# Kernel tuning notes

Measured on AMD Instinct MI355X. Metric: run time of the kernel, lower is better.

Reference implementation:

```python
import jax, jax.numpy as jnp
import numpy as np

VOXEL_SIZE = 0.05  # from init_kwargs


def _voxel_ds(pts, voxel_size, key, L):
    """Voxel-grid downsample one cloud (N,3): mean of points per occupied voxel,
    then resample L voxel centroids (uniform with replacement among valid voxels).
    Static shapes throughout (jit/vmap friendly)."""
    N = pts.shape[0]
    mn = jnp.min(pts, axis=0)
    v = jnp.floor((pts - mn) / voxel_size).astype(jnp.int32)      # (N,3) voxel coords >= 0
    dims = jnp.max(v, axis=0) + 1                                  # traced grid extents
    lin = (v[:, 0] * dims[1] + v[:, 1]) * dims[2] + v[:, 2]        # linearized voxel id
    order = jnp.argsort(lin)
    sl = lin[order]
    is_new = jnp.concatenate([jnp.ones((1,), bool), sl[1:] != sl[:-1]])
    seg = jnp.cumsum(is_new) - 1                                   # compact segment id per sorted point
    num_vox = seg[-1] + 1                                          # traced count of occupied voxels
    sums = jax.ops.segment_sum(pts[order], seg, num_segments=N)    # (N,3) padded
    cnt = jax.ops.segment_sum(jnp.ones((N,), pts.dtype), seg, num_segments=N)
    means = sums / jnp.maximum(cnt, 1.0)[:, None]                  # voxel centroids
    # random resample L centroids among the first num_vox valid segments
    u = jax.random.uniform(key, (L,))
    idx = jnp.minimum((u * num_vox.astype(u.dtype)).astype(jnp.int32), num_vox - 1)
    return means[idx]                                              # (L,3)


def _voxel_layer(x, voxel_size, L, key):
    # x: (B,3,N) -> (B,3,L)
    B = x.shape[0]
    pts = jnp.transpose(x, (0, 2, 1))                              # (B,N,3)
    keys = jax.random.split(key, B)
    out = jax.vmap(lambda p, k: _voxel_ds(p, voxel_size, k, L))(pts, keys)
    return jnp.transpose(out, (0, 2, 1))                           # (B,3,L)


def setup_inputs() -> dict:
    key = jax.random.key(0)
    x = jax.random.uniform(key, (16, 3, 262144), dtype=jnp.float32)
    return {"x": x}


def reference(x):
    B, _, N = x.shape
    L1, L2 = N // 2, N // 4
    k1, k2 = jax.random.split(jax.random.key(42))
    voxel_x1 = _voxel_layer(x, VOXEL_SIZE, L1, k1)
    voxel_x2 = _voxel_layer(voxel_x1, 2.0 * VOXEL_SIZE, L2, k2)
    return (voxel_x1, voxel_x2)
```

## Files before the change

### kernel.cpp

```cpp
#include <hip/hip_runtime.h>
#include <stdint.h>


typedef unsigned int u32;
typedef unsigned long long u64;

struct KeyArr { uint32_t k0[16]; uint32_t k1[16]; };

__host__ __device__ inline void tf2x32(uint32_t k0, uint32_t k1,
                                       uint32_t c0, uint32_t c1,
                                       uint32_t& o0, uint32_t& o1) {
  const uint32_t ks0 = k0, ks1 = k1, ks2 = k0 ^ k1 ^ 0x1BD11BDAu;
  uint32_t x0 = c0 + ks0, x1 = c1 + ks1;
#define TF_R(r) { x0 += x1; x1 = (x1 << (r)) | (x1 >> (32 - (r))); x1 ^= x0; }
  TF_R(13) TF_R(15) TF_R(26) TF_R(6)
  x0 += ks1; x1 += ks2 + 1u;
  TF_R(17) TF_R(29) TF_R(16) TF_R(24)
  x0 += ks2; x1 += ks0 + 2u;
  TF_R(13) TF_R(15) TF_R(26) TF_R(6)
  x0 += ks0; x1 += ks1 + 3u;
  TF_R(17) TF_R(29) TF_R(16) TF_R(24)
  x0 += ks1; x1 += ks2 + 4u;
  TF_R(13) TF_R(15) TF_R(26) TF_R(6)
  x0 += ks2; x1 += ks0 + 5u;
#undef TF_R
  o0 = x0; o1 = x1;
}

__global__ void init_kernel(u64* cellsA, u64* cellsB, int ncells) {
  int i = blockIdx.x * blockDim.x + threadIdx.x;
  int stride = gridDim.x * blockDim.x;
  for (int j = i; j < ncells; j += stride) { cellsA[j] = 0ull; cellsB[j] = 0ull; }
}

__global__ void min_kernel(const float* __restrict__ in, int n4,
                           float* __restrict__ pmin) {
  int row = blockIdx.y;
  int PB = gridDim.x;
  const float4* p = (const float4*)in + (size_t)row * n4;
  int base = blockIdx.x * 2048 + threadIdx.x;
  float4 v0 = p[base];
  float4 v1 = p[base + 256];
  float4 v2 = p[base + 512];
  float4 v3 = p[base + 768];
  float4 v4 = p[base + 1024];
  float4 v5 = p[base + 1280];
  float4 v6 = p[base + 1536];
  float4 v7 = p[base + 1792];
  float m0 = fminf(fminf(v0.x, v0.y), fminf(v0.z, v0.w));
  float m1 = fminf(fminf(v1.x, v1.y), fminf(v1.z, v1.w));
  float m2 = fminf(fminf(v2.x, v2.y), fminf(v2.z, v2.w));
  float m3 = fminf(fminf(v3.x, v3.y), fminf(v3.z, v3.w));
  float m4 = fminf(fminf(v4.x, v4.y), fminf(v4.z, v4.w));
  float m5 = fminf(fminf(v5.x, v5.y), fminf(v5.z, v5.w));
  float m6 = fminf(fminf(v6.x, v6.y), fminf(v6.z, v6.w));
  float m7 = fminf(fminf(v7.x, v7.y), fminf(v7.z, v7.w));
  float m = fminf(fminf(fminf(m0, m1), fminf(m2, m3)),
                  fminf(fminf(m4, m5), fminf(m6, m7)));
  for (int off = 32; off > 0; off >>= 1)
    m = fminf(m, __shfl_down(m, off, 64));
  __shared__ float wmin[4];
  int wid = threadIdx.x >> 6;
  if ((threadIdx.x & 63) == 0) wmin[wid] = m;
  __syncthreads();
  if (threadIdx.x == 0)
    pmin[row * PB + blockIdx.x] =
        fminf(fminf(wmin[0], wmin[1]), fminf(wmin[2], wmin[3]));
}

template <int G, int S, bool ATOMIC>
__global__ __launch_bounds__(1024) void accum_kernel(
    const float* __restrict__ in, int N, float vox,
    const float* __restrict__ pmin, int PB, u64* __restrict__ Ap,
    u64* __restrict__ Bp) {
  extern __shared__ u64 lds[];
  u64* lA = lds;
  u64* lB = lds + G;
  __shared__ float s_m[3];
  int tid = threadIdx.x, b = blockIdx.y;
  for (int i = tid; i < G; i += 1024) { lA[i] = 0ull; lB[i] = 0ull; }

  int wid = tid >> 6, lane = tid & 63;
  if (wid < 3) {
    float v = __int_as_float(0x7F800000);
    for (int j = lane; j < PB; j += 64)
      v = fminf(v, pmin[(b * 3 + wid) * PB + j]);
    for (int off = 32; off > 0; off >>= 1)
      v = fminf(v, __shfl_down(v, off, 64));
    if (lane == 0) s_m[wid] = v;
  }
  __syncthreads();
  float m0 = s_m[0], m1 = s_m[1], m2 = s_m[2];

  int ppb = N / gridDim.x;
  const float* base = in + (size_t)b * 3 * N;
  int start = blockIdx.x * ppb;
  const float4* r0 = (const float4*)(base + start);
  const float4* r1 = (const float4*)(base + N + start);
  const float4* r2 = (const float4*)(base + 2 * N + start);
  int q4 = ppb >> 2;
  for (int i = tid; i < q4; i += 1024) {
    float4 X = r0[i], Y = r1[i], Z = r2[i];
#define PT(px, py, pz) { \
    int v0 = (int)floorf(((px) - m0) / vox); \
    int v1 = (int)floorf(((py) - m1) / vox); \
    int v2 = (int)floorf(((pz) - m2) / vox); \
    int lin = (v0 * S + v1) * S + v2; \
    u32 qx = (u32)((px) * 1048576.0f); \
    u32 qy = (u32)((py) * 1048576.0f); \
    u32 qz = (u32)((pz) * 1048576.0f); \
    atomicAdd(&lA[lin], ((u64)qy << 32) | (u64)qx); \
    atomicAdd(&lB[lin], (1ull << 32) | (u64)qz); }
    PT(X.x, Y.x, Z.x) PT(X.y, Y.y, Z.y) PT(X.z, Y.z, Z.z) PT(X.w, Y.w, Z.w)
#undef PT
  }
  __syncthreads();

  int p = ATOMIC ? 0 : blockIdx.x;
  u64* gA = Ap + ((size_t)p * 16 + b) * G;
  u64* gB = Bp + ((size_t)p * 16 + b) * G;
  for (int c = tid; c < G; c += 1024) {
    if (ATOMIC) {
      u64 Bv = lB[c];
      if (Bv) { atomicAdd(&gA[c], lA[c]); atomicAdd(&gB[c], Bv); }
    } else {
      gA[c] = lA[c];
      gB[c] = lB[c];
    }
  }
}

__global__ void reduce_kernel(int G, int P, const u64* __restrict__ Ap,
                              const u64* __restrict__ Bp,
                              float4* __restrict__ vox4,
                              u32* __restrict__ bcnt) {
  int blk = blockIdx.x, b = blockIdx.y, tid = threadIdx.x;
  int cell = blk * 256 + tid;
  u64 A = 0ull, Bv = 0ull;
  if (cell < G) {
    for (int p = 0; p < P; ++p) {
      size_t o = ((size_t)p * 16 + b) * G + cell;
      A += Ap[o];
      Bv += Bp[o];
    }
  }
  u32 cnt = (u32)(Bv >> 32);
  if (cell < G) {
    float4 o4 = make_float4(0.f, 0.f, 0.f, 0.f);
    if (cnt) {
      double inv = 1.0 / (1048576.0 * (double)cnt);
      o4.x = (float)((double)(u32)A * inv);
      o4.y = (float)((double)(u32)(A >> 32) * inv);
      o4.z = (float)((double)(u32)Bv * inv);
      o4.w = (float)cnt;
    }
    vox4[(size_t)b * G + cell] = o4;
  }
  u64 mask = __ballot(cnt > 0u);
  __shared__ u32 wtot[4];
  if ((tid & 63) == 0) wtot[tid >> 6] = (u32)__popcll(mask);
  __syncthreads();
  if (tid == 0)
    bcnt[b * gridDim.x + blk] = wtot[0] + wtot[1] + wtot[2] + wtot[3];
}

__global__ void compact_b_kernel(int G, const float4* __restrict__ vox4,
                                 const u32* __restrict__ bcnt,
                                 float4* __restrict__ means4,
                                 u32* __restrict__ numvox) {
  int blk = blockIdx.x, nb = gridDim.x, b = blockIdx.y, tid = threadIdx.x;
  int lane = tid & 63, wid = tid >> 6;
  int cell = blk * 256 + tid;
  float4 v = make_float4(0.f, 0.f, 0.f, 0.f);
  bool occ = false;
  if (cell < G) {
    v = vox4[(size_t)b * G + cell];
    occ = v.w > 0.f;
  }
  u64 mask = __ballot(occ);
  u32 prefix = (u32)__popcll(mask & ((1ull << lane) - 1ull));
  __shared__ u32 wb[4];
  if (lane == 0) wb[wid] = (u32)__popcll(mask);
  __syncthreads();
  if (tid == 0) {
    u32 base = 0;
    for (int j = 0; j < blk; ++j) base += bcnt[b * nb + j];
    u32 s = base;
    for (int w = 0; w < 4; ++w) { u32 t = wb[w]; wb[w] = s; s += t; }
    if (blk == nb - 1) numvox[b] = s;
  }
  __syncthreads();
  if (occ) means4[(size_t)b * G + wb[wid] + prefix] = v;
}

template <int G>
__global__ __launch_bounds__(1024) void redcomp_kernel(
    int P, const u64* __restrict__ Ap, const u64* __restrict__ Bp,
    float4* __restrict__ means4, u32* __restrict__ numvox) {
  int b = blockIdx.x, tid = threadIdx.x, wid = tid >> 6, lane = tid & 63;
  u64 A = 0ull, Bv = 0ull;
  if (tid < G) {
    for (int p = 0; p < P; ++p) {
      size_t o = ((size_t)p * 16 + b) * G + tid;
      A += Ap[o];
      Bv += Bp[o];
    }
  }
  u32 cnt = (u32)(Bv >> 32);
  float4 v = make_float4(0.f, 0.f, 0.f, 0.f);
  if (cnt) {
    double inv = 1.0 / (1048576.0 * (double)cnt);
    v.x = (float)((double)(u32)A * inv);
    v.y = (float)((double)(u32)(A >> 32) * inv);
    v.z = (float)((double)(u32)Bv * inv);
  }
  bool occ = cnt > 0u;
  u64 mask = __ballot(occ);
  u32 prefix = (u32)__popcll(mask & ((1ull << lane) - 1ull));
  __shared__ u32 wtot[16], wbase[16];
  if (lane == 0) wtot[wid] = (u32)__popcll(mask);
  __syncthreads();
  if (tid == 0) {
    u32 s = 0;
    for (int w = 0; w < 16; ++w) { wbase[w] = s; s += wtot[w]; }
    numvox[b] = s;
  }
  __syncthreads();
  if (occ) means4[(size_t)b * G + wbase[wid] + prefix] = v;
}

__global__ __launch_bounds__(1024) void compact_kernel(
    int G, const u64* __restrict__ Ac, const u64* __restrict__ Bc,
    float4* __restrict__ means4, u32* __restrict__ numvox) {
  int b = blockIdx.x, tid = threadIdx.x, wid = tid >> 6, lane = tid & 63;
  __shared__ u32 wtot[16], wbase[16];
  __shared__ u32 gbase;
  if (tid == 0) gbase = 0u;
  __syncthreads();
  for (int t0 = 0; t0 < G; t0 += 1024) {
    int cell = t0 + tid;
    float4 v = make_float4(0.f, 0.f, 0.f, 0.f);
    u32 cnt = 0u;
    if (cell < G) {
      u64 A = Ac[(size_t)b * G + cell], Bv = Bc[(size_t)b * G + cell];
      cnt = (u32)(Bv >> 32);
      if (cnt) {
        double inv = 1.0 / (1048576.0 * (double)cnt);
        v.x = (float)((double)(u32)A * inv);
        v.y = (float)((double)(u32)(A >> 32) * inv);
        v.z = (float)((double)(u32)Bv * inv);
      }
    }
    bool occ = cnt > 0u;
    u64 mask = __ballot(occ);
    u32 prefix = (u32)__popcll(mask & ((1ull << lane) - 1ull));
    if (lane == 0) wtot[wid] = (u32)__popcll(mask);
    __syncthreads();
    if (tid == 0) {
      u32 s = gbase;
      for (int w = 0; w < 16; ++w) { wbase[w] = s; s += wtot[w]; }
      gbase = s;
    }
    __syncthreads();
    if (occ) means4[(size_t)b * G + wbase[wid] + prefix] = v;
    __syncthreads();
  }
  if (tid == 0) numvox[b] = gbase;
}

template <bool DOMIN>
__global__ void sample_kernel(int L, int G, const float4* __restrict__ means4,
                              const u32* __restrict__ numvox, KeyArr keys,
                              float* __restrict__ out,
                              float* __restrict__ pmin) {
  int t = blockIdx.x * 256 + threadIdx.x;
  int b = blockIdx.y;
  int l0 = t * 4;
  u32 nv = numvox[b];
  float fnv = (float)nv;
  int nvm1 = (int)nv - 1;
  uint32_t K0 = keys.k0[b], K1 = keys.k1[b];
  float4 m[4];
#pragma unroll
  for (int j = 0; j < 4; ++j) {
    uint32_t w0, w1;
    tf2x32(K0, K1, 0u, (uint32_t)(l0 + j), w0, w1);
    uint32_t bits = w0 ^ w1;
    float u = __uint_as_float((bits >> 9) | 0x3F800000u) - 1.0f;
    int idx = (int)(u * fnv);
    if (idx > nvm1) idx = nvm1;
    m[j] = means4[(size_t)b * G + idx];
  }
  *(float4*)(out + ((size_t)b * 3 + 0) * L + l0) =
      make_float4(m[0].x, m[1].x, m[2].x, m[3].x);
  *(float4*)(out + ((size_t)b * 3 + 1) * L + l0) =
      make_float4(m[0].y, m[1].y, m[2].y, m[3].y);
  *(float4*)(out + ((size_t)b * 3 + 2) * L + l0) =
      make_float4(m[0].z, m[1].z, m[2].z, m[3].z);
  if (DOMIN) {
    float ax = fminf(fminf(m[0].x, m[1].x), fminf(m[2].x, m[3].x));
    float ay = fminf(fminf(m[0].y, m[1].y), fminf(m[2].y, m[3].y));
    float az = fminf(fminf(m[0].z, m[1].z), fminf(m[2].z, m[3].z));
    for (int off = 32; off > 0; off >>= 1) {
      ax = fminf(ax, __shfl_down(ax, off, 64));
      ay = fminf(ay, __shfl_down(ay, off, 64));
      az = fminf(az, __shfl_down(az, off, 64));
    }
    __shared__ float wm[4][3];
    int wid = threadIdx.x >> 6;
    if ((threadIdx.x & 63) == 0) {
      wm[wid][0] = ax; wm[wid][1] = ay; wm[wid][2] = az;
    }
    __syncthreads();
    if (threadIdx.x == 0) {
      int PB = gridDim.x;
      pmin[(b * 3 + 0) * PB + blockIdx.x] =
          fminf(fminf(wm[0][0], wm[1][0]), fminf(wm[2][0], wm[3][0]));
      pmin[(b * 3 + 1) * PB + blockIdx.x] =
          fminf(fminf(wm[0][1], wm[1][1]), fminf(wm[2][1], wm[3][1]));
      pmin[(b * 3 + 2) * PB + blockIdx.x] =
          fminf(fminf(wm[0][2], wm[1][2]), fminf(wm[2][2], wm[3][2]));
    }
  }
}

extern "C" void kernel_launch(void* const* d_in, const int* in_sizes, int n_in,
                              void* d_out, int out_size, void* d_ws,
                              size_t ws_size, hipStream_t stream) {
  const float* x = (const float*)d_in[0];
  float* out = (float*)d_out;

  uint32_t k1a, k1b, k2a, k2b;
  tf2x32(0u, 42u, 0u, 0u, k1a, k1b);
  tf2x32(0u, 42u, 0u, 1u, k2a, k2b);
  KeyArr keys1, keys2;
  for (int b = 0; b < 16; ++b) {
    tf2x32(k1a, k1b, 0u, (uint32_t)b, keys1.k0[b], keys1.k1[b]);
    tf2x32(k2a, k2b, 0u, (uint32_t)b, keys2.k0[b], keys2.k1[b]);
  }

  const int N1 = 262144, L1 = 131072, L2 = 65536, G1 = 8000, G2 = 1000;
  const int PB1 = 32, PB2 = 128, NB1 = 32;
  const size_t slice1 = (size_t)16 * G1, slice2 = (size_t)16 * G2;

  const size_t tailBytes =
      (48 * PB1 + 48 * PB2 + 16 * NB1 + 32) * 4 + 256;
  const size_t bigNeed =
      2ull * 16 * slice1 * 8 + 2ull * slice1 * 16 + tailBytes;
  bool big = ws_size >= bigNeed;

  uint8_t* w = (uint8_t*)d_ws;
  u64 *Ap, *Bp;
  float4 *vox4 = nullptr, *means4;
  uint8_t* tail;
  if (big) {
    Ap = (u64*)w;
    Bp = Ap + 16 * slice1;
    vox4 = (float4*)(Bp + 16 * slice1);
    means4 = vox4 + slice1;
    tail = (uint8_t*)(means4 + slice1);
  } else {
    Ap = (u64*)w;
    Bp = Ap + (slice1 + slice2);
    means4 = (float4*)(Bp + (slice1 + slice2));
    tail = (uint8_t*)(means4 + slice1);
  }
  float* pmin1 = (float*)tail;
  float* pmin2 = pmin1 + 48 * PB1;
  u32* bcnt = (u32*)(pmin2 + 48 * PB2);
  u32* numvox = bcnt + 16 * NB1;

  if (!big) {
    init_kernel<<<dim3(64), dim3(256), 0, stream>>>(
        Ap, Bp, (int)(slice1 + slice2));
  }

  min_kernel<<<dim3(PB1, 48), dim3(256), 0, stream>>>(x, N1 / 4, pmin1);
  if (big) {
    accum_kernel<G1, 20, false>
        <<<dim3(16, 16), dim3(1024), 2 * G1 * 8, stream>>>(x, N1, 0.05f,
                                                           pmin1, PB1, Ap, Bp);
    reduce_kernel<<<dim3(NB1, 16), dim3(256), 0, stream>>>(G1, 16, Ap, Bp,
                                                           vox4, bcnt);
    compact_b_kernel<<<dim3(NB1, 16), dim3(256), 0, stream>>>(
        G1, vox4, bcnt, means4, numvox);
  } else {
    accum_kernel<G1, 20, true>
        <<<dim3(8, 16), dim3(1024), 2 * G1 * 8, stream>>>(x, N1, 0.05f, pmin1,
                                                          PB1, Ap, Bp);
    compact_kernel<<<dim3(16), dim3(1024), 0, stream>>>(G1, Ap, Bp, means4,
                                                        numvox);
  }
  sample_kernel<true><<<dim3(L1 / 1024, 16), dim3(256), 0, stream>>>(
      L1, G1, means4, numvox, keys1, out, pmin2);

  float* out2 = out + (size_t)48 * L1;
  if (big) {
    accum_kernel<G2, 10, false>
        <<<dim3(16, 16), dim3(1024), 2 * G2 * 8, stream>>>(
            out, L1, 0.1f, pmin2, PB2, Ap, Bp);
    redcomp_kernel<G2><<<dim3(16), dim3(1024), 0, stream>>>(
        16, Ap, Bp, means4, numvox + 16);
  } else {
    accum_kernel<G2, 10, true>
        <<<dim3(8, 16), dim3(1024), 2 * G2 * 8, stream>>>(
            out, L1, 0.1f, pmin2, PB2, Ap + slice1, Bp + slice1);
    compact_kernel<<<dim3(16), dim3(1024), 0, stream>>>(
        G2, Ap + slice1, Bp + slice1, means4, numvox + 16);
  }
  sample_kernel<false><<<dim3(L2 / 1024, 16), dim3(256), 0, stream>>>(
      L2, G2, means4, numvox + 16, keys2, out2, nullptr);
}
```

Measured before the change: 71.92 us.

## Fuse stage-1 reduce and compaction into per-chunk compaction with chunked sampling

Replaces the separate reduce and compact kernels for the first layer with one kernel. It sums the 16 partial grids and compacts occupied voxels independently within 16 chunks of 500 cells per batch, writing per-chunk counts. A new sampling kernel builds the prefix of chunk counts in registers and maps each random index to its chunk and offset. This removes a kernel launch, the intermediate vox4 round-trip and the serial block-prefix loop, at the cost of a small per-sample chunk search.

```diff
diff --git a/kernel.cpp b/kernel.cpp
--- a/kernel.cpp
+++ b/kernel.cpp
@@ -27,6 +27,26 @@
   o0 = x0; o1 = x1;
 }
 
+#define MN1 262144
+#define ML1 131072
+#define ML2 65536
+#define MG1 8000
+#define MG2 1000
+
+__device__ __forceinline__ void bin1(float px, float py, float pz, float m0,
+                                     float m1, float m2, float vox, int S,
+                                     u64* lA, u64* lB) {
+  int v0 = (int)floorf((px - m0) / vox);
+  int v1 = (int)floorf((py - m1) / vox);
+  int v2 = (int)floorf((pz - m2) / vox);
+  int lin = (v0 * S + v1) * S + v2;
+  u32 qx = (u32)(px * 1048576.0f);
+  u32 qy = (u32)(py * 1048576.0f);
+  u32 qz = (u32)(pz * 1048576.0f);
+  atomicAdd(&lA[lin], ((u64)qy << 32) | (u64)qx);
+  atomicAdd(&lB[lin], (1ull << 32) | (u64)qz);
+}
+
 __global__ void init_kernel(u64* cellsA, u64* cellsB, int ncells) {
   int i = blockIdx.x * blockDim.x + threadIdx.x;
   int stride = gridDim.x * blockDim.x;
@@ -39,14 +59,9 @@
   int PB = gridDim.x;
   const float4* p = (const float4*)in + (size_t)row * n4;
   int base = blockIdx.x * 2048 + threadIdx.x;
-  float4 v0 = p[base];
-  float4 v1 = p[base + 256];
-  float4 v2 = p[base + 512];
-  float4 v3 = p[base + 768];
-  float4 v4 = p[base + 1024];
-  float4 v5 = p[base + 1280];
-  float4 v6 = p[base + 1536];
-  float4 v7 = p[base + 1792];
+  float4 v0 = p[base], v1 = p[base + 256], v2 = p[base + 512],
+         v3 = p[base + 768], v4 = p[base + 1024], v5 = p[base + 1280],
+         v6 = p[base + 1536], v7 = p[base + 1792];
   float m0 = fminf(fminf(v0.x, v0.y), fminf(v0.z, v0.w));
   float m1 = fminf(fminf(v1.x, v1.y), fminf(v1.z, v1.w));
   float m2 = fminf(fminf(v2.x, v2.y), fminf(v2.z, v2.w));
@@ -79,7 +94,6 @@
   __shared__ float s_m[3];
   int tid = threadIdx.x, b = blockIdx.y;
   for (int i = tid; i < G; i += 1024) { lA[i] = 0ull; lB[i] = 0ull; }
-
   int wid = tid >> 6, lane = tid & 63;
   if (wid < 3) {
     float v = __int_as_float(0x7F800000);
@@ -91,7 +105,6 @@
   }
   __syncthreads();
   float m0 = s_m[0], m1 = s_m[1], m2 = s_m[2];
-
   int ppb = N / gridDim.x;
   const float* base = in + (size_t)b * 3 * N;
   int start = blockIdx.x * ppb;
@@ -101,21 +114,12 @@
   int q4 = ppb >> 2;
   for (int i = tid; i < q4; i += 1024) {
     float4 X = r0[i], Y = r1[i], Z = r2[i];
-#define PT(px, py, pz) { \
-    int v0 = (int)floorf(((px) - m0) / vox); \
-    int v1 = (int)floorf(((py) - m1) / vox); \
-    int v2 = (int)floorf(((pz) - m2) / vox); \
-    int lin = (v0 * S + v1) * S + v2; \
-    u32 qx = (u32)((px) * 1048576.0f); \
-    u32 qy = (u32)((py) * 1048576.0f); \
-    u32 qz = (u32)((pz) * 1048576.0f); \
-    atomicAdd(&lA[lin], ((u64)qy << 32) | (u64)qx); \
-    atomicAdd(&lB[lin], (1ull << 32) | (u64)qz); }
-    PT(X.x, Y.x, Z.x) PT(X.y, Y.y, Z.y) PT(X.z, Y.z, Z.z) PT(X.w, Y.w, Z.w)
-#undef PT
-  }
-  __syncthreads();
-
+    bin1(X.x, Y.x, Z.x, m0, m1, m2, vox, S, lA, lB);
+    bin1(X.y, Y.y, Z.y, m0, m1, m2, vox, S, lA, lB);
+    bin1(X.z, Y.z, Z.z, m0, m1, m2, vox, S, lA, lB);
+    bin1(X.w, Y.w, Z.w, m0, m1, m2, vox, S, lA, lB);
+  }
+  __syncthreads();
   int p = ATOMIC ? 0 : blockIdx.x;
   u64* gA = Ap + ((size_t)p * 16 + b) * G;
   u64* gB = Bp + ((size_t)p * 16 + b) * G;
@@ -130,67 +134,107 @@
   }
 }
 
-__global__ void reduce_kernel(int G, int P, const u64* __restrict__ Ap,
-                              const u64* __restrict__ Bp,
-                              float4* __restrict__ vox4,
-                              u32* __restrict__ bcnt) {
-  int blk = blockIdx.x, b = blockIdx.y, tid = threadIdx.x;
-  int cell = blk * 256 + tid;
-  u64 A = 0ull, Bv = 0ull;
-  if (cell < G) {
-    for (int p = 0; p < P; ++p) {
-      size_t o = ((size_t)p * 16 + b) * G + cell;
+__global__ __launch_bounds__(512) void redcomp1_kernel(
+    const u64* __restrict__ Ap, const u64* __restrict__ Bp,
+    float4* __restrict__ mc1 , u32* __restrict__ ccnt1) {
+  int c = blockIdx.x, b = blockIdx.y;
+  int tid = threadIdx.x, lane = tid & 63, wid = tid >> 6;
+  __shared__ u32 s_w[16];
+  float4 v = make_float4(0.f, 0.f, 0.f, 0.f);
+  bool occ = false;
+  if (tid < 500) {
+    int cell = c * 500 + tid;
+    u64 A = 0ull, Bv = 0ull;
+#pragma unroll
+    for (int p = 0; p < 16; ++p) {
+      size_t o = ((size_t)p * 16 + b) * MG1 + cell;
       A += Ap[o];
       Bv += Bp[o];
     }
-  }
-  u32 cnt = (u32)(Bv >> 32);
-  if (cell < G) {
-    float4 o4 = make_float4(0.f, 0.f, 0.f, 0.f);
+    u32 cnt = (u32)(Bv >> 32);
     if (cnt) {
       double inv = 1.0 / (1048576.0 * (double)cnt);
-      o4.x = (float)((double)(u32)A * inv);
-      o4.y = (float)((double)(u32)(A >> 32) * inv);
-      o4.z = (float)((double)(u32)Bv * inv);
-      o4.w = (float)cnt;
-    }
-    vox4[(size_t)b * G + cell] = o4;
-  }
-  u64 mask = __ballot(cnt > 0u);
-  __shared__ u32 wtot[4];
-  if ((tid & 63) == 0) wtot[tid >> 6] = (u32)__popcll(mask);
-  __syncthreads();
-  if (tid == 0)
-    bcnt[b * gridDim.x + blk] = wtot[0] + wtot[1] + wtot[2] + wtot[3];
-}
-
-__global__ void compact_b_kernel(int G, const float4* __restrict__ vox4,
-                                 const u32* __restrict__ bcnt,
-                                 float4* __restrict__ means4,
-                                 u32* __restrict__ numvox) {
-  int blk = blockIdx.x, nb = gridDim.x, b = blockIdx.y, tid = threadIdx.x;
-  int lane = tid & 63, wid = tid >> 6;
-  int cell = blk * 256 + tid;
-  float4 v = make_float4(0.f, 0.f, 0.f, 0.f);
-  bool occ = false;
-  if (cell < G) {
-    v = vox4[(size_t)b * G + cell];
-    occ = v.w > 0.f;
+      v.x = (float)((double)(u32)A * inv);
+      v.y = (float)((double)(u32)(A >> 32) * inv);
+      v.z = (float)((double)(u32)Bv * inv);
+      occ = true;
+    }
   }
   u64 mask = __ballot(occ);
-  u32 prefix = (u32)__popcll(mask & ((1ull << lane) - 1ull));
-  __shared__ u32 wb[4];
-  if (lane == 0) wb[wid] = (u32)__popcll(mask);
+  u32 wpre = (u32)__popcll(mask & ((1ull << lane) - 1ull));
+  if (lane == 0) s_w[wid] = (u32)__popcll(mask);
   __syncthreads();
   if (tid == 0) {
-    u32 base = 0;
-    for (int j = 0; j < blk; ++j) base += bcnt[b * nb + j];
-    u32 s = base;
-    for (int w = 0; w < 4; ++w) { u32 t = wb[w]; wb[w] = s; s += t; }
-    if (blk == nb - 1) numvox[b] = s;
-  }
-  __syncthreads();
-  if (occ) means4[(size_t)b * G + wb[wid] + prefix] = v;
+    u32 s = 0;
+    for (int w = 0; w < 8; ++w) { u32 t = s_w[w]; s_w[8 + w] = s; s += t; }
+    ccnt1[b * 16 + c] = s;
+  }
+  __syncthreads();
+  if (occ) mc1[((size_t)b * 16 + c) * 500 + s_w[8 + wid] + wpre] = v;
+}
+
+__global__ void sample1_kernel(const float4* __restrict__ mc1,
+                               const u32* __restrict__ ccnt1, KeyArr keys,
+                               float* __restrict__ out,
+                               float* __restrict__ pmin2) {
+  int t = blockIdx.x * 256 + threadIdx.x;
+  int b = blockIdx.y;
+  int l0 = t * 4;
+  u32 pre[17];
+  pre[0] = 0u;
+#pragma unroll
+  for (int j = 0; j < 16; ++j) pre[j + 1] = pre[j] + ccnt1[b * 16 + j];
+  u32 nv = pre[16];
+  float fnv = (float)nv;
+  int nvm1 = (int)nv - 1;
+  uint32_t K0 = keys.k0[b], K1 = keys.k1[b];
+  float4 m[4];
+#pragma unroll
+  for (int j = 0; j < 4; ++j) {
+    uint32_t w0, w1;
+    tf2x32(K0, K1, 0u, (uint32_t)(l0 + j), w0, w1);
+    uint32_t bits = w0 ^ w1;
+    float u = __uint_as_float((bits >> 9) | 0x3F800000u) - 1.0f;
+    int idx = (int)(u * fnv);
+    if (idx > nvm1) idx = nvm1;
+    int ch = 0;
+    u32 base = 0u;
+#pragma unroll
+    for (int q = 1; q < 16; ++q) {
+      u32 pq = pre[q];
+      if ((u32)idx >= pq) { ch = q; base = pq; }
+    }
+    m[j] = mc1[((size_t)b * 16 + ch) * 500 + (idx - (int)base)];
+  }
+  *(float4*)(out + ((size_t)b * 3 + 0) * ML1 + l0) =
+      make_float4(m[0].x, m[1].x, m[2].x, m[3].x);
+  *(float4*)(out + ((size_t)b * 3 + 1) * ML1 + l0) =
+      make_float4(m[0].y, m[1].y, m[2].y, m[3].y);
+  *(float4*)(out + ((size_t)b * 3 + 2) * ML1 + l0) =
+      make_float4(m[0].z, m[1].z, m[2].z, m[3].z);
+  float ax = fminf(fminf(m[0].x, m[1].x), fminf(m[2].x, m[3].x));
+  float ay = fminf(fminf(m[0].y, m[1].y), fminf(m[2].y, m[3].y));
+  float az = fminf(fminf(m[0].z, m[1].z), fminf(m[2].z, m[3].z));
+  for (int off = 32; off > 0; off >>= 1) {
+    ax = fminf(ax, __shfl_down(ax, off, 64));
+    ay = fminf(ay, __shfl_down(ay, off, 64));
+    az = fminf(az, __shfl_down(az, off, 64));
+  }
+  __shared__ float wm[4][3];
+  int wid = threadIdx.x >> 6;
+  if ((threadIdx.x & 63) == 0) {
+    wm[wid][0] = ax; wm[wid][1] = ay; wm[wid][2] = az;
+  }
+  __syncthreads();
+  if (threadIdx.x == 0) {
+    int PB = gridDim.x;
+    pmin2[(b * 3 + 0) * PB + blockIdx.x] =
+        fminf(fminf(wm[0][0], wm[1][0]), fminf(wm[2][0], wm[3][0]));
+    pmin2[(b * 3 + 1) * PB + blockIdx.x] =
+        fminf(fminf(wm[0][1], wm[1][1]), fminf(wm[2][1], wm[3][1]));
+    pmin2[(b * 3 + 2) * PB + blockIdx.x] =
+        fminf(fminf(wm[0][2], wm[1][2]), fminf(wm[2][2], wm[3][2]));
+  }
 }
 
 template <int G>
@@ -227,45 +271,6 @@
   }
   __syncthreads();
   if (occ) means4[(size_t)b * G + wbase[wid] + prefix] = v;
-}
-
-__global__ __launch_bounds__(1024) void compact_kernel(
-    int G, const u64* __restrict__ Ac, const u64* __restrict__ Bc,
-    float4* __restrict__ means4, u32* __restrict__ numvox) {
-  int b = blockIdx.x, tid = threadIdx.x, wid = tid >> 6, lane = tid & 63;
-  __shared__ u32 wtot[16], wbase[16];
-  __shared__ u32 gbase;
-  if (tid == 0) gbase = 0u;
-  __syncthreads();
-  for (int t0 = 0; t0 < G; t0 += 1024) {
-    int cell = t0 + tid;
-    float4 v = make_float4(0.f, 0.f, 0.f, 0.f);
-    u32 cnt = 0u;
-    if (cell < G) {
-      u64 A = Ac[(size_t)b * G + cell], Bv = Bc[(size_t)b * G + cell];
-      cnt = (u32)(Bv >> 32);
-      if (cnt) {
-        double inv = 1.0 / (1048576.0 * (double)cnt);
-        v.x = (float)((double)(u32)A * inv);
-        v.y = (float)((double)(u32)(A >> 32) * inv);
-        v.z = (float)((double)(u32)Bv * inv);
-      }
-    }
-    bool occ = cnt > 0u;
-    u64 mask = __ballot(occ);
-    u32 prefix = (u32)__popcll(mask & ((1ull << lane) - 1ull));
-    if (lane == 0) wtot[wid] = (u32)__popcll(mask);
-    __syncthreads();
-    if (tid == 0) {
-      u32 s = gbase;
-      for (int w = 0; w < 16; ++w) { wbase[w] = s; s += wtot[w]; }
-      gbase = s;
-    }
-    __syncthreads();
-    if (occ) means4[(size_t)b * G + wbase[wid] + prefix] = v;
-    __syncthreads();
-  }
-  if (tid == 0) numvox[b] = gbase;
 }
 
 template <bool DOMIN>
@@ -324,6 +329,45 @@
   }
 }
 
+__global__ __launch_bounds__(1024) void compact_kernel(
+    int G, const u64* __restrict__ Ac, const u64* __restrict__ Bc,
+    float4* __restrict__ means4, u32* __restrict__ numvox) {
+  int b = blockIdx.x, tid = threadIdx.x, wid = tid >> 6, lane = tid & 63;
+  __shared__ u32 wtot[16], wbase[16];
+  __shared__ u32 gbase;
+  if (tid == 0) gbase = 0u;
+  __syncthreads();
+  for (int t0 = 0; t0 < G; t0 += 1024) {
+    int cell = t0 + tid;
+    float4 v = make_float4(0.f, 0.f, 0.f, 0.f);
+    u32 cnt = 0u;
+    if (cell < G) {
+      u64 A = Ac[(size_t)b * G + cell], Bv = Bc[(size_t)b * G + cell];
+      cnt = (u32)(Bv >> 32);
+      if (cnt) {
+        double inv = 1.0 / (1048576.0 * (double)cnt);
+        v.x = (float)((double)(u32)A * inv);
+        v.y = (float)((double)(u32)(A >> 32) * inv);
+        v.z = (float)((double)(u32)Bv * inv);
+      }
+    }
+    bool occ = cnt > 0u;
+    u64 mask = __ballot(occ);
+    u32 prefix = (u32)__popcll(mask & ((1ull << lane) - 1ull));
+    if (lane == 0) wtot[wid] = (u32)__popcll(mask);
+    __syncthreads();
+    if (tid == 0) {
+      u32 s = gbase;
+      for (int w = 0; w < 16; ++w) { wbase[w] = s; s += wtot[w]; }
+      gbase = s;
+    }
+    __syncthreads();
+    if (occ) means4[(size_t)b * G + wbase[wid] + prefix] = v;
+    __syncthreads();
+  }
+  if (tid == 0) numvox[b] = gbase;
+}
+
 extern "C" void kernel_launch(void* const* d_in, const int* in_sizes, int n_in,
                               void* d_out, int out_size, void* d_ws,
                               size_t ws_size, hipStream_t stream) {
@@ -339,75 +383,71 @@
     tf2x32(k2a, k2b, 0u, (uint32_t)b, keys2.k0[b], keys2.k1[b]);
   }
 
-  const int N1 = 262144, L1 = 131072, L2 = 65536, G1 = 8000, G2 = 1000;
-  const int PB1 = 32, PB2 = 128, NB1 = 32;
-  const size_t slice1 = (size_t)16 * G1, slice2 = (size_t)16 * G2;
-
-  const size_t tailBytes =
-      (48 * PB1 + 48 * PB2 + 16 * NB1 + 32) * 4 + 256;
-  const size_t bigNeed =
-      2ull * 16 * slice1 * 8 + 2ull * slice1 * 16 + tailBytes;
-  bool big = ws_size >= bigNeed;
+  const int PB1 = 32, PB2 = 128;
+  const size_t oAp = 0;
+  const size_t oBp = oAp + (size_t)16 * 16 * MG1 * 8;
+  const size_t oMc1 = oBp + (size_t)16 * 16 * MG1 * 8;
+  const size_t oMc2 = oMc1 + (size_t)16 * 16 * 500 * 16;
+  const size_t oPm1 = oMc2 + (size_t)16 * MG2 * 16;
+  const size_t oPm2 = oPm1 + 48 * PB1 * 4;
+  const size_t oCc1 = oPm2 + 48 * PB2 * 4;
+  const size_t oNv = oCc1 + 256 * 4;
+  const size_t bigNeed = oNv + 128;
 
   uint8_t* w = (uint8_t*)d_ws;
-  u64 *Ap, *Bp;
-  float4 *vox4 = nullptr, *means4;
-  uint8_t* tail;
-  if (big) {
-    Ap = (u64*)w;
-    Bp = Ap + 16 * slice1;
-    vox4 = (float4*)(Bp + 16 * slice1);
-    means4 = vox4 + slice1;
-    tail = (uint8_t*)(means4 + slice1);
-  } else {
-    Ap = (u64*)w;
-    Bp = Ap + (slice1 + slice2);
-    means4 = (float4*)(Bp + (slice1 + slice2));
-    tail = (uint8_t*)(means4 + slice1);
-  }
-  float* pmin1 = (float*)tail;
-  float* pmin2 = pmin1 + 48 * PB1;
-  u32* bcnt = (u32*)(pmin2 + 48 * PB2);
-  u32* numvox = bcnt + 16 * NB1;
-
-  if (!big) {
-    init_kernel<<<dim3(64), dim3(256), 0, stream>>>(
-        Ap, Bp, (int)(slice1 + slice2));
-  }
-
-  min_kernel<<<dim3(PB1, 48), dim3(256), 0, stream>>>(x, N1 / 4, pmin1);
-  if (big) {
-    accum_kernel<G1, 20, false>
-        <<<dim3(16, 16), dim3(1024), 2 * G1 * 8, stream>>>(x, N1, 0.05f,
-                                                           pmin1, PB1, Ap, Bp);
-    reduce_kernel<<<dim3(NB1, 16), dim3(256), 0, stream>>>(G1, 16, Ap, Bp,
-                                                           vox4, bcnt);
-    compact_b_kernel<<<dim3(NB1, 16), dim3(256), 0, stream>>>(
-        G1, vox4, bcnt, means4, numvox);
-  } else {
-    accum_kernel<G1, 20, true>
-        <<<dim3(8, 16), dim3(1024), 2 * G1 * 8, stream>>>(x, N1, 0.05f, pmin1,
-                                                          PB1, Ap, Bp);
-    compact_kernel<<<dim3(16), dim3(1024), 0, stream>>>(G1, Ap, Bp, means4,
-                                                        numvox);
-  }
-  sample_kernel<true><<<dim3(L1 / 1024, 16), dim3(256), 0, stream>>>(
-      L1, G1, means4, numvox, keys1, out, pmin2);
-
-  float* out2 = out + (size_t)48 * L1;
-  if (big) {
-    accum_kernel<G2, 10, false>
-        <<<dim3(16, 16), dim3(1024), 2 * G2 * 8, stream>>>(
-            out, L1, 0.1f, pmin2, PB2, Ap, Bp);
-    redcomp_kernel<G2><<<dim3(16), dim3(1024), 0, stream>>>(
-        16, Ap, Bp, means4, numvox + 16);
-  } else {
-    accum_kernel<G2, 10, true>
-        <<<dim3(8, 16), dim3(1024), 2 * G2 * 8, stream>>>(
-            out, L1, 0.1f, pmin2, PB2, Ap + slice1, Bp + slice1);
-    compact_kernel<<<dim3(16), dim3(1024), 0, stream>>>(
-        G2, Ap + slice1, Bp + slice1, means4, numvox + 16);
-  }
-  sample_kernel<false><<<dim3(L2 / 1024, 16), dim3(256), 0, stream>>>(
-      L2, G2, means4, numvox + 16, keys2, out2, nullptr);
-}
+  if (ws_size >= bigNeed) {
+    u64* Ap = (u64*)(w + oAp);
+    u64* Bp = (u64*)(w + oBp);
+    float4* mc1 = (float4*)(w + oMc1);
+    float4* mc2 = (float4*)(w + oMc2);
+    float* pmin1 = (float*)(w + oPm1);
+    float* pmin2 = (float*)(w + oPm2);
+    u32* ccnt1 = (u32*)(w + oCc1);
+    u32* numvox2 = (u32*)(w + oNv);
+
+    min_kernel<<<dim3(PB1, 48), dim3(256), 0, stream>>>(x, MN1 / 4, pmin1);
+    accum_kernel<MG1, 20, false>
+        <<<dim3(16, 16), dim3(1024), 2 * MG1 * 8, stream>>>(x, MN1, 0.05f,
+                                                            pmin1, PB1, Ap, Bp);
+    redcomp1_kernel<<<dim3(16, 16), dim3(512), 0, stream>>>(Ap, Bp, mc1,
+                                                            ccnt1);
+    sample1_kernel<<<dim3(ML1 / 1024, 16), dim3(256), 0, stream>>>(
+        mc1, ccnt1, keys1, out, pmin2);
+    float* out2 = out + (size_t)48 * ML1;
+    accum_kernel<MG2, 10, false>
+        <<<dim3(16, 16), dim3(1024), 2 * MG2 * 8, stream>>>(
+            out, ML1, 0.1f, pmin2, PB2, Ap, Bp);
+    redcomp_kernel<MG2><<<dim3(16), dim3(1024), 0, stream>>>(16, Ap, Bp, mc2,
+                                                             numvox2);
+    sample_kernel<false><<<dim3(ML2 / 1024, 16), dim3(256), 0, stream>>>(
+        ML2, MG2, mc2, numvox2, keys2, out2, nullptr);
+    return;
+  }
+
+  const size_t slice1 = (size_t)16 * MG1, slice2 = (size_t)16 * MG2;
+  u64* As = (u64*)w;
+  u64* Bs = As + (slice1 + slice2);
+  float4* means4s = (float4*)(Bs + (slice1 + slice2));
+  float* pmin1s = (float*)(means4s + slice1);
+  float* pmin2s = pmin1s + 48 * PB1;
+  u32* numvoxs = (u32*)(pmin2s + 48 * PB2);
+
+  init_kernel<<<dim3(64), dim3(256), 0, stream>>>(As, Bs,
+                                                  (int)(slice1 + slice2));
+  min_kernel<<<dim3(PB1, 48), dim3(256), 0, stream>>>(x, MN1 / 4, pmin1s);
+  accum_kernel<MG1, 20, true>
+      <<<dim3(8, 16), dim3(1024), 2 * MG1 * 8, stream>>>(x, MN1, 0.05f, pmin1s,
+                                                         PB1, As, Bs);
+  compact_kernel<<<dim3(16), dim3(1024), 0, stream>>>(MG1, As, Bs, means4s,
+                                                      numvoxs);
+  sample_kernel<true><<<dim3(ML1 / 1024, 16), dim3(256), 0, stream>>>(
+      ML1, MG1, means4s, numvoxs, keys1, out, pmin2s);
+  float* out2 = out + (size_t)48 * ML1;
+  accum_kernel<MG2, 10, true>
+      <<<dim3(8, 16), dim3(1024), 2 * MG2 * 8, stream>>>(
+          out, ML1, 0.1f, pmin2s, PB2, As + slice1, Bs + slice1);
+  compact_kernel<<<dim3(16), dim3(1024), 0, stream>>>(
+      MG2, As + slice1, Bs + slice1, means4s, numvoxs + 16);
+  sample_kernel<false><<<dim3(ML2 / 1024, 16), dim3(256), 0, stream>>>(
+      ML2, MG2, means4s, numvoxs + 16, keys2, out2, nullptr);
+}
```

Result: faster. 68.76 us (-4.4%).
